# Kernel tuning notes

Measured on AMD Instinct MI355X. Metric: run time of the kernel, lower is better.

Reference implementation:

```python
import jax, jax.numpy as jnp
import numpy as np

ALPHA = 0.1  # LeakyReLU slope

def _leaky(v):
    return jnp.where(v >= 0, v, ALPHA * v)

def setup_inputs() -> dict:
    key = jax.random.key(0)
    k1, k2, k3 = jax.random.split(key, 3)
    B, D_IN, D1, D2 = 262144, 200, 150, 100
    x = jax.random.normal(k1, (B, D_IN), dtype=jnp.float32)
    W1 = jax.random.normal(k2, (D_IN, D1), dtype=jnp.float32) * 0.05
    b1 = jnp.zeros((D1,), dtype=jnp.float32)
    W2 = jax.random.normal(k3, (D1, D2), dtype=jnp.float32) * 0.05
    b2 = jnp.zeros((D2,), dtype=jnp.float32)
    return {"x": x, "W1": W1, "b1": b1, "W2": W2, "b2": b2}

def reference(x, W1, b1, W2, b2):
    # Original loops per sample: dense(200->150)+LeakyReLU, mean -> out1;
    # dense(150->100)+LeakyReLU, mean -> out2. Batched here as single GEMMs.
    h1 = _leaky(x @ W1 + b1)           # [B, 150]
    out1 = jnp.mean(h1, axis=-1)       # [B]
    h2 = _leaky(h1 @ W2 + b2)          # [B, 100]
    out2 = jnp.mean(h2, axis=-1)       # [B]
    return (out1, out2)
```

## Files before the change

kernel.cpp:

```cpp
#include <hip/hip_runtime.h>

typedef unsigned short u16;
typedef unsigned int u32;
typedef __bf16 bf16x8 __attribute__((ext_vector_type(8)));
typedef float f32x4 __attribute__((ext_vector_type(4)));

#define W2F_OFF 71680
#define B1_OFF 107520
#define B2_OFF 108160
#define WS_BYTES 108608

__device__ __align__(256) unsigned char g_wbuf[WS_BYTES];

__device__ __forceinline__ u16 f2bf(float f) {
  __bf16 b = (__bf16)f;
  return __builtin_bit_cast(u16, b);
}
__device__ __forceinline__ u32 pk2bf(float a, float b) {
  return (u32)f2bf(a) | ((u32)f2bf(b) << 16);
}

__global__ void prep_kernel(const float* __restrict__ W1, const float* __restrict__ b1,
                            const float* __restrict__ W2, const float* __restrict__ b2)
{
  const int stride = gridDim.x * blockDim.x;
  const int tid0 = blockIdx.x * blockDim.x + threadIdx.x;
  u16* w1f = (u16*)g_wbuf;
  for (int e = tid0; e < 35840; e += stride) {
    int j = e & 7, l = (e >> 3) & 63, nt = (e >> 9) % 10, kt = e / 5120;
    int k = kt * 32 + ((l >> 4) << 3) + j;
    int n = nt * 16 + (l & 15);
    w1f[e] = (k < 200 && n < 150) ? f2bf(W1[k * 150 + n]) : (u16)0;
  }
  u16* w2f = (u16*)(g_wbuf + W2F_OFF);
  for (int e = tid0; e < 17920; e += stride) {
    int j = e & 7, l = (e >> 3) & 63, nt = (e >> 9) % 7, kt = e / 3584;
    int k = kt * 32 + ((l >> 4) << 3) + j;
    int n = nt * 16 + (l & 15);
    w2f[e] = (k < 150 && n < 100) ? f2bf(W2[k * 100 + n]) : (u16)0;
  }
  float* b1p = (float*)(g_wbuf + B1_OFF);
  for (int e = tid0; e < 160; e += stride) b1p[e] = (e < 150) ? b1[e] : 0.f;
  float* b2p = (float*)(g_wbuf + B2_OFF);
  for (int e = tid0; e < 112; e += stride) b2p[e] = (e < 100) ? b2[e] : 0.f;
}

__device__ __forceinline__ void stage_write(u16* __restrict__ xs, int c, float4 v) {
  int row = c / 50, kc = c % 50;
  int k0 = kc * 4, mt = row >> 4;
  int idx;
  if (k0 < 192) {
    int F = mt * 6 + (k0 >> 5);
    int fl = (row & 15) | (((k0 & 31) >> 3) << 4);
    idx = (F * 64 + (fl ^ (F & 7))) * 8 + (k0 & 7);
  } else {
    idx = 12288 + mt * 128 + (row & 15) * 8 + (k0 - 192);
  }
  uint2 p;
  p.x = pk2bf(v.x, v.y);
  p.y = pk2bf(v.z, v.w);
  *reinterpret_cast<uint2*>(&xs[idx]) = p;
}

#define NT 8
#define SMEM_BYTES 159744

__global__ __launch_bounds__(512, 2)
void fused_mlp(const float* __restrict__ x, float* __restrict__ out, int B)
{
  extern __shared__ __align__(16) u16 smem[];
  u16* wlds = smem;
  float* ps = (float*)(smem + 79360);

  const int tid = threadIdx.x;
  const int lane = tid & 63;
  const int wv = tid >> 6;
  const int h = wv & 1;
  const int mt = wv >> 1;
  const int cl = lane & 15, gr = lane >> 4;

  {
    const uint4* src = (const uint4*)g_wbuf;
    uint4* dst = (uint4*)wlds;
    #pragma unroll
    for (int i = 0; i < 14; ++i) {
      int c = tid + i * 512;
      if (c < 6720) dst[c] = src[c];
    }
  }

  const float* b1p = (const float*)(g_wbuf + B1_OFF);
  const float* b2p = (const float*)(g_wbuf + B2_OFF);
  float b1v[5];
  #pragma unroll
  for (int nt = 0; nt < 5; ++nt) b1v[nt] = b1p[(5 * h + nt) * 16 + cl];
  float b2v[4];
  #pragma unroll
  for (int nt = 0; nt < 4; ++nt)
    b2v[nt] = (nt < 3 || h == 0) ? b2p[(4 * h + nt) * 16 + cl] : 0.f;

  const long rowBase = (long)blockIdx.x * (NT * 64);
  const f32x4 zz = {0.f, 0.f, 0.f, 0.f};

  float4 rv[7];
  {
    const float* xg = x + rowBase * 200;
    #pragma unroll
    for (int i = 0; i < 7; ++i) {
      int c = tid + i * 512;
      rv[i] = (c < 3200) ? *reinterpret_cast<const float4*>(xg + (c / 50) * 200 + (c % 50) * 4)
                         : make_float4(0.f, 0.f, 0.f, 0.f);
    }
    u16* x0 = smem + 53760;
    #pragma unroll
    for (int i = 0; i < 7; ++i) {
      int c = tid + i * 512;
      if (c < 3200) stage_write(x0, c, rv[i]);
    }
  }
  __syncthreads();

  for (int t = 0; t < NT; ++t) {
    u16* xcur = smem + 53760 + (t & 1) * 12800;
    u16* xnxt = smem + 53760 + ((t + 1) & 1) * 12800;
    const long r0t = rowBase + (long)t * 64;

    if (t + 1 < NT) {
      const float* xg = x + (r0t + 64) * 200;
      #pragma unroll
      for (int i = 0; i < 7; ++i) {
        int c = tid + i * 512;
        rv[i] = (c < 3200) ? *reinterpret_cast<const float4*>(xg + (c / 50) * 200 + (c % 50) * 4)
                           : make_float4(0.f, 0.f, 0.f, 0.f);
      }
    }

    f32x4 acc1[5];
    #pragma unroll
    for (int nt = 0; nt < 5; ++nt) acc1[nt] = zz;

    #pragma unroll
    for (int kt = 0; kt < 7; ++kt) {
      bf16x8 a;
      if (kt < 6) {
        int F = mt * 6 + kt;
        a = *reinterpret_cast<const bf16x8*>(&xcur[(F * 64 + (lane ^ (F & 7))) * 8]);
      } else {
        union { bf16x8 v; u32 w[4]; } A;
        A.v = *reinterpret_cast<const bf16x8*>(&xcur[12288 + mt * 128 + cl * 8]);
        if (gr != 0) { A.w[0] = A.w[1] = A.w[2] = A.w[3] = 0u; }
        a = A.v;
      }
      #pragma unroll
      for (int nt = 0; nt < 5; ++nt) {
        bf16x8 b = *reinterpret_cast<const bf16x8*>(&wlds[((kt * 10 + 5 * h + nt) * 64 + lane) * 8]);
        acc1[nt] = __builtin_amdgcn_mfma_f32_16x16x32_bf16(a, b, acc1[nt], 0, 0, 0);
      }
    }
    __syncthreads();

    float rs[4] = {0, 0, 0, 0};
    #pragma unroll
    for (int nt = 0; nt < 5; ++nt) {
      int k2 = (5 * h + nt) * 16 + cl;
      int kt2 = k2 >> 5;
      int l2base = 16 * ((k2 & 31) >> 3);
      int e2 = k2 & 7;
      #pragma unroll
      for (int j = 0; j < 4; ++j) {
        int l2 = gr * 4 + j + l2base;
        float hv = acc1[nt][j] + b1v[nt];
        hv = (hv >= 0.f) ? hv : 0.1f * hv;
        rs[j] += hv;
        xcur[((mt * 5 + kt2) * 64 + l2) * 8 + e2] = f2bf(hv);
      }
    }
    #pragma unroll
    for (int j = 0; j < 4; ++j) {
      float s = rs[j];
      #pragma unroll
      for (int mask = 1; mask < 16; mask <<= 1) s += __shfl_xor(s, mask, 64);
      if (cl == 0) ps[h * 64 + mt * 16 + gr * 4 + j] = s;
    }
    __syncthreads();

    if (tid < 64)
      out[r0t + tid] = (ps[tid] + ps[64 + tid]) * (1.f / 150.f);

    f32x4 acc2[4];
    #pragma unroll
    for (int nt = 0; nt < 4; ++nt) acc2[nt] = zz;

    #pragma unroll
    for (int kt = 0; kt < 5; ++kt) {
      bf16x8 a = *reinterpret_cast<const bf16x8*>(&xcur[((mt * 5 + kt) * 64 + lane) * 8]);
      #pragma unroll
      for (int nt = 0; nt < 4; ++nt) {
        if (nt < 3 || h == 0) {
          bf16x8 b = *reinterpret_cast<const bf16x8*>(&wlds[35840 + ((kt * 7 + 4 * h + nt) * 64 + lane) * 8]);
          acc2[nt] = __builtin_amdgcn_mfma_f32_16x16x32_bf16(a, b, acc2[nt], 0, 0, 0);
        }
      }
    }

    float ts[4] = {0, 0, 0, 0};
    #pragma unroll
    for (int nt = 0; nt < 4; ++nt) {
      if (nt < 3 || h == 0) {
        #pragma unroll
        for (int j = 0; j < 4; ++j) {
          float hv = acc2[nt][j] + b2v[nt];
          hv = (hv >= 0.f) ? hv : 0.1f * hv;
          ts[j] += hv;
        }
      }
    }
    #pragma unroll
    for (int j = 0; j < 4; ++j) {
      float s = ts[j];
      #pragma unroll
      for (int mask = 1; mask < 16; mask <<= 1) s += __shfl_xor(s, mask, 64);
      if (cl == 0) ps[128 + h * 64 + mt * 16 + gr * 4 + j] = s;
    }

    if (t + 1 < NT) {
      #pragma unroll
      for (int i = 0; i < 7; ++i) {
        int c = tid + i * 512;
        if (c < 3200) stage_write(xnxt, c, rv[i]);
      }
    }
    __syncthreads();

    if (tid < 64)
      out[B + r0t + tid] = (ps[128 + tid] + ps[192 + tid]) * (1.f / 100.f);
  }
}

extern "C" void kernel_launch(void* const* d_in, const int* in_sizes, int n_in,
                              void* d_out, int out_size, void* d_ws, size_t ws_size,
                              hipStream_t stream)
{
  const float* x  = (const float*)d_in[0];
  const float* W1 = (const float*)d_in[1];
  const float* b1 = (const float*)d_in[2];
  const float* W2 = (const float*)d_in[3];
  const float* b2 = (const float*)d_in[4];
  float* out = (float*)d_out;
  const int B = in_sizes[0] / 200;

  hipFuncSetAttribute(reinterpret_cast<const void*>(fused_mlp),
                      hipFuncAttributeMaxDynamicSharedMemorySize, SMEM_BYTES);

  prep_kernel<<<64, 256, 0, stream>>>(W1, b1, W2, b2);
  fused_mlp<<<B / (NT * 64), 512, SMEM_BYTES, stream>>>(x, out, B);
}
```

Measured before the change: 88.87 us.

## Drop LDS weight staging; read weights from global/L2 with one tile per block

Each block now handles a single 64-row tile instead of looping over 8 tiles with a double-buffered x stage. The weights are read directly from the global workspace, with register prefetch of the next k-slice, instead of being copied into a large LDS buffer. This shrinks LDS to about 26KB so more blocks fit per CU (launch bounds raised to 5), and it removes the per-block weight copy. In exchange, weight fragments are re-read from L2 by every block, and the cross-tile overlap of x loads with compute is gone.

```diff
diff --git a/kernel.cpp b/kernel.cpp
--- a/kernel.cpp
+++ b/kernel.cpp
@@ -45,32 +45,11 @@
   for (int e = tid0; e < 112; e += stride) b2p[e] = (e < 100) ? b2[e] : 0.f;
 }
 
-__device__ __forceinline__ void stage_write(u16* __restrict__ xs, int c, float4 v) {
-  int row = c / 50, kc = c % 50;
-  int k0 = kc * 4, mt = row >> 4;
-  int idx;
-  if (k0 < 192) {
-    int F = mt * 6 + (k0 >> 5);
-    int fl = (row & 15) | (((k0 & 31) >> 3) << 4);
-    idx = (F * 64 + (fl ^ (F & 7))) * 8 + (k0 & 7);
-  } else {
-    idx = 12288 + mt * 128 + (row & 15) * 8 + (k0 - 192);
-  }
-  uint2 p;
-  p.x = pk2bf(v.x, v.y);
-  p.y = pk2bf(v.z, v.w);
-  *reinterpret_cast<uint2*>(&xs[idx]) = p;
-}
-
-#define NT 8
-#define SMEM_BYTES 159744
-
-__global__ __launch_bounds__(512, 2)
+__global__ __launch_bounds__(512, 5)
 void fused_mlp(const float* __restrict__ x, float* __restrict__ out, int B)
 {
-  extern __shared__ __align__(16) u16 smem[];
-  u16* wlds = smem;
-  float* ps = (float*)(smem + 79360);
+  __shared__ __align__(16) u16 xs[12800];
+  __shared__ float ps[2][2][64];
 
   const int tid = threadIdx.x;
   const int lane = tid & 63;
@@ -78,163 +57,153 @@
   const int h = wv & 1;
   const int mt = wv >> 1;
   const int cl = lane & 15, gr = lane >> 4;
-
-  {
-    const uint4* src = (const uint4*)g_wbuf;
-    uint4* dst = (uint4*)wlds;
-    #pragma unroll
-    for (int i = 0; i < 14; ++i) {
-      int c = tid + i * 512;
-      if (c < 6720) dst[c] = src[c];
-    }
-  }
+  const long r0 = (long)blockIdx.x * 64;
+
+  const u16* w1g = (const u16*)g_wbuf;
+  const u16* w2g = (const u16*)(g_wbuf + W2F_OFF);
+
+  const float* xg = x + r0 * 200;
+  #pragma unroll
+  for (int i = 0; i < 7; ++i) {
+    int c = tid + i * 512;
+    if (c < 3200) {
+      int row = c / 50, kc = c % 50;
+      float4 v = *reinterpret_cast<const float4*>(xg + row * 200 + kc * 4);
+      int k0 = kc * 4;
+      int m = row >> 4;
+      int idx;
+      if (k0 < 192) {
+        int F = m * 6 + (k0 >> 5);
+        int fl = (row & 15) | (((k0 & 31) >> 3) << 4);
+        idx = (F * 64 + (fl ^ (F & 7))) * 8 + (k0 & 7);
+      } else {
+        idx = 12288 + m * 128 + (row & 15) * 8 + (k0 - 192);
+      }
+      uint2 p;
+      p.x = pk2bf(v.x, v.y);
+      p.y = pk2bf(v.z, v.w);
+      *reinterpret_cast<uint2*>(&xs[idx]) = p;
+    }
+  }
+
+  bf16x8 bfr[5];
+  #pragma unroll
+  for (int nt = 0; nt < 5; ++nt)
+    bfr[nt] = *reinterpret_cast<const bf16x8*>(w1g + ((0 * 10 + 5 * h + nt) * 64 + lane) * 8);
+
+  __syncthreads();
+
+  const f32x4 zz = {0.f, 0.f, 0.f, 0.f};
+  f32x4 acc1[5];
+  #pragma unroll
+  for (int nt = 0; nt < 5; ++nt) acc1[nt] = zz;
+
+  #pragma unroll
+  for (int kt = 0; kt < 7; ++kt) {
+    bf16x8 bnx[5];
+    if (kt < 6) {
+      #pragma unroll
+      for (int nt = 0; nt < 5; ++nt)
+        bnx[nt] = *reinterpret_cast<const bf16x8*>(w1g + (((kt + 1) * 10 + 5 * h + nt) * 64 + lane) * 8);
+    }
+    bf16x8 a;
+    if (kt < 6) {
+      int F = mt * 6 + kt;
+      a = *reinterpret_cast<const bf16x8*>(&xs[(F * 64 + (lane ^ (F & 7))) * 8]);
+    } else {
+      union { bf16x8 v; u32 w[4]; } A;
+      A.v = *reinterpret_cast<const bf16x8*>(&xs[12288 + mt * 128 + cl * 8]);
+      if (gr != 0) { A.w[0] = A.w[1] = A.w[2] = A.w[3] = 0u; }
+      a = A.v;
+    }
+    #pragma unroll
+    for (int nt = 0; nt < 5; ++nt)
+      acc1[nt] = __builtin_amdgcn_mfma_f32_16x16x32_bf16(a, bfr[nt], acc1[nt], 0, 0, 0);
+    if (kt < 6) {
+      #pragma unroll
+      for (int nt = 0; nt < 5; ++nt) bfr[nt] = bnx[nt];
+    }
+  }
+  __syncthreads();
 
   const float* b1p = (const float*)(g_wbuf + B1_OFF);
+  float b1v[5];
+  #pragma unroll
+  for (int nt = 0; nt < 5; ++nt) b1v[nt] = b1p[(5 * h + nt) * 16 + cl];
+
+  float rs[4] = {0, 0, 0, 0};
+  #pragma unroll
+  for (int nt = 0; nt < 5; ++nt) {
+    int k2 = (5 * h + nt) * 16 + cl;
+    int kt2 = k2 >> 5;
+    int l2base = 16 * ((k2 & 31) >> 3);
+    int e2 = k2 & 7;
+    #pragma unroll
+    for (int j = 0; j < 4; ++j) {
+      int l2 = gr * 4 + j + l2base;
+      float hv = acc1[nt][j] + b1v[nt];
+      hv = (hv >= 0.f) ? hv : 0.1f * hv;
+      rs[j] += hv;
+      xs[((mt * 5 + kt2) * 64 + l2) * 8 + e2] = f2bf(hv);
+    }
+  }
+  #pragma unroll
+  for (int j = 0; j < 4; ++j) {
+    float s = rs[j];
+    #pragma unroll
+    for (int mask = 1; mask < 16; mask <<= 1) s += __shfl_xor(s, mask, 64);
+    if (cl == 0) ps[0][h][mt * 16 + gr * 4 + j] = s;
+  }
+  __syncthreads();
+
+  if (tid < 64)
+    out[r0 + tid] = (ps[0][0][tid] + ps[0][1][tid]) * (1.f / 150.f);
+
+  f32x4 acc2[4];
+  #pragma unroll
+  for (int nt = 0; nt < 4; ++nt) acc2[nt] = zz;
+
+  #pragma unroll
+  for (int kt = 0; kt < 5; ++kt) {
+    bf16x8 a = *reinterpret_cast<const bf16x8*>(&xs[((mt * 5 + kt) * 64 + lane) * 8]);
+    #pragma unroll
+    for (int nt = 0; nt < 4; ++nt) {
+      if (nt < 3 || h == 0) {
+        bf16x8 b = *reinterpret_cast<const bf16x8*>(w2g + ((kt * 7 + 4 * h + nt) * 64 + lane) * 8);
+        acc2[nt] = __builtin_amdgcn_mfma_f32_16x16x32_bf16(a, b, acc2[nt], 0, 0, 0);
+      }
+    }
+  }
+
   const float* b2p = (const float*)(g_wbuf + B2_OFF);
-  float b1v[5];
-  #pragma unroll
-  for (int nt = 0; nt < 5; ++nt) b1v[nt] = b1p[(5 * h + nt) * 16 + cl];
   float b2v[4];
   #pragma unroll
   for (int nt = 0; nt < 4; ++nt)
     b2v[nt] = (nt < 3 || h == 0) ? b2p[(4 * h + nt) * 16 + cl] : 0.f;
 
-  const long rowBase = (long)blockIdx.x * (NT * 64);
-  const f32x4 zz = {0.f, 0.f, 0.f, 0.f};
-
-  float4 rv[7];
-  {
-    const float* xg = x + rowBase * 200;
-    #pragma unroll
-    for (int i = 0; i < 7; ++i) {
-      int c = tid + i * 512;
-      rv[i] = (c < 3200) ? *reinterpret_cast<const float4*>(xg + (c / 50) * 200 + (c % 50) * 4)
-                         : make_float4(0.f, 0.f, 0.f, 0.f);
-    }
-    u16* x0 = smem + 53760;
-    #pragma unroll
-    for (int i = 0; i < 7; ++i) {
-      int c = tid + i * 512;
-      if (c < 3200) stage_write(x0, c, rv[i]);
-    }
-  }
-  __syncthreads();
-
-  for (int t = 0; t < NT; ++t) {
-    u16* xcur = smem + 53760 + (t & 1) * 12800;
-    u16* xnxt = smem + 53760 + ((t + 1) & 1) * 12800;
-    const long r0t = rowBase + (long)t * 64;
-
-    if (t + 1 < NT) {
-      const float* xg = x + (r0t + 64) * 200;
-      #pragma unroll
-      for (int i = 0; i < 7; ++i) {
-        int c = tid + i * 512;
-        rv[i] = (c < 3200) ? *reinterpret_cast<const float4*>(xg + (c / 50) * 200 + (c % 50) * 4)
-                           : make_float4(0.f, 0.f, 0.f, 0.f);
-      }
-    }
-
-    f32x4 acc1[5];
-    #pragma unroll
-    for (int nt = 0; nt < 5; ++nt) acc1[nt] = zz;
-
-    #pragma unroll
-    for (int kt = 0; kt < 7; ++kt) {
-      bf16x8 a;
-      if (kt < 6) {
-        int F = mt * 6 + kt;
-        a = *reinterpret_cast<const bf16x8*>(&xcur[(F * 64 + (lane ^ (F & 7))) * 8]);
-      } else {
-        union { bf16x8 v; u32 w[4]; } A;
-        A.v = *reinterpret_cast<const bf16x8*>(&xcur[12288 + mt * 128 + cl * 8]);
-        if (gr != 0) { A.w[0] = A.w[1] = A.w[2] = A.w[3] = 0u; }
-        a = A.v;
-      }
-      #pragma unroll
-      for (int nt = 0; nt < 5; ++nt) {
-        bf16x8 b = *reinterpret_cast<const bf16x8*>(&wlds[((kt * 10 + 5 * h + nt) * 64 + lane) * 8]);
-        acc1[nt] = __builtin_amdgcn_mfma_f32_16x16x32_bf16(a, b, acc1[nt], 0, 0, 0);
-      }
-    }
-    __syncthreads();
-
-    float rs[4] = {0, 0, 0, 0};
-    #pragma unroll
-    for (int nt = 0; nt < 5; ++nt) {
-      int k2 = (5 * h + nt) * 16 + cl;
-      int kt2 = k2 >> 5;
-      int l2base = 16 * ((k2 & 31) >> 3);
-      int e2 = k2 & 7;
+  float ts[4] = {0, 0, 0, 0};
+  #pragma unroll
+  for (int nt = 0; nt < 4; ++nt) {
+    if (nt < 3 || h == 0) {
       #pragma unroll
       for (int j = 0; j < 4; ++j) {
-        int l2 = gr * 4 + j + l2base;
-        float hv = acc1[nt][j] + b1v[nt];
+        float hv = acc2[nt][j] + b2v[nt];
         hv = (hv >= 0.f) ? hv : 0.1f * hv;
-        rs[j] += hv;
-        xcur[((mt * 5 + kt2) * 64 + l2) * 8 + e2] = f2bf(hv);
+        ts[j] += hv;
       }
     }
-    #pragma unroll
-    for (int j = 0; j < 4; ++j) {
-      float s = rs[j];
-      #pragma unroll
-      for (int mask = 1; mask < 16; mask <<= 1) s += __shfl_xor(s, mask, 64);
-      if (cl == 0) ps[h * 64 + mt * 16 + gr * 4 + j] = s;
-    }
-    __syncthreads();
-
-    if (tid < 64)
-      out[r0t + tid] = (ps[tid] + ps[64 + tid]) * (1.f / 150.f);
-
-    f32x4 acc2[4];
-    #pragma unroll
-    for (int nt = 0; nt < 4; ++nt) acc2[nt] = zz;
-
-    #pragma unroll
-    for (int kt = 0; kt < 5; ++kt) {
-      bf16x8 a = *reinterpret_cast<const bf16x8*>(&xcur[((mt * 5 + kt) * 64 + lane) * 8]);
-      #pragma unroll
-      for (int nt = 0; nt < 4; ++nt) {
-        if (nt < 3 || h == 0) {
-          bf16x8 b = *reinterpret_cast<const bf16x8*>(&wlds[35840 + ((kt * 7 + 4 * h + nt) * 64 + lane) * 8]);
-          acc2[nt] = __builtin_amdgcn_mfma_f32_16x16x32_bf16(a, b, acc2[nt], 0, 0, 0);
-        }
-      }
-    }
-
-    float ts[4] = {0, 0, 0, 0};
-    #pragma unroll
-    for (int nt = 0; nt < 4; ++nt) {
-      if (nt < 3 || h == 0) {
-        #pragma unroll
-        for (int j = 0; j < 4; ++j) {
-          float hv = acc2[nt][j] + b2v[nt];
-          hv = (hv >= 0.f) ? hv : 0.1f * hv;
-          ts[j] += hv;
-        }
-      }
-    }
-    #pragma unroll
-    for (int j = 0; j < 4; ++j) {
-      float s = ts[j];
-      #pragma unroll
-      for (int mask = 1; mask < 16; mask <<= 1) s += __shfl_xor(s, mask, 64);
-      if (cl == 0) ps[128 + h * 64 + mt * 16 + gr * 4 + j] = s;
-    }
-
-    if (t + 1 < NT) {
-      #pragma unroll
-      for (int i = 0; i < 7; ++i) {
-        int c = tid + i * 512;
-        if (c < 3200) stage_write(xnxt, c, rv[i]);
-      }
-    }
-    __syncthreads();
-
-    if (tid < 64)
-      out[B + r0t + tid] = (ps[128 + tid] + ps[192 + tid]) * (1.f / 100.f);
-  }
+  }
+  #pragma unroll
+  for (int j = 0; j < 4; ++j) {
+    float s = ts[j];
+    #pragma unroll
+    for (int mask = 1; mask < 16; mask <<= 1) s += __shfl_xor(s, mask, 64);
+    if (cl == 0) ps[1][h][mt * 16 + gr * 4 + j] = s;
+  }
+  __syncthreads();
+
+  if (tid < 64)
+    out[B + r0 + tid] = (ps[1][0][tid] + ps[1][1][tid]) * (1.f / 100.f);
 }
 
 extern "C" void kernel_launch(void* const* d_in, const int* in_sizes, int n_in,
@@ -249,9 +218,6 @@
   float* out = (float*)d_out;
   const int B = in_sizes[0] / 200;
 
-  hipFuncSetAttribute(reinterpret_cast<const void*>(fused_mlp),
-                      hipFuncAttributeMaxDynamicSharedMemorySize, SMEM_BYTES);
-
   prep_kernel<<<64, 256, 0, stream>>>(W1, b1, W2, b2);
-  fused_mlp<<<B / (NT * 64), 512, SMEM_BYTES, stream>>>(x, out, B);
-}
+  fused_mlp<<<B / 64, 512, 0, stream>>>(x, out, B);
+}
```

Result: faster. 85.27 us (-4.1%).
